# Kernel optimization log

Measured on AMD Instinct MI355X. Metric: run time of the kernel, lower is better.

Reference implementation:

```python
import jax, jax.numpy as jnp
import numpy as np


def setup_inputs() -> dict:
    key = jax.random.key(0)
    ks = jax.random.split(key, 8)
    C = 256
    Cq = C // 8  # 32
    B, H, W = 4, 64, 64
    x = jax.random.normal(ks[0], (B, C, H, W), dtype=jnp.float32)
    wq = jax.random.normal(ks[1], (Cq, C), dtype=jnp.float32) * (1.0 / np.sqrt(C))
    bq = jax.random.normal(ks[2], (Cq,), dtype=jnp.float32) * 0.01
    wk = jax.random.normal(ks[3], (Cq, C), dtype=jnp.float32) * (1.0 / np.sqrt(C))
    bk = jax.random.normal(ks[4], (Cq,), dtype=jnp.float32) * 0.01
    wv = jax.random.normal(ks[5], (C, C), dtype=jnp.float32) * (1.0 / np.sqrt(C))
    bv = jax.random.normal(ks[6], (C,), dtype=jnp.float32) * 0.01
    gamma = jax.random.normal(ks[7], (1,), dtype=jnp.float32)
    return {"x": x, "wq": wq, "bq": bq, "wk": wk, "bk": bk,
            "wv": wv, "bv": bv, "gamma": gamma}


def reference(x, wq, bq, wk, bk, wv, bv, gamma):
    B, C, H, W = x.shape
    N = H * W
    xf = x.reshape(B, C, N)  # [B, C, N] flattened spatial
    # 1x1 convs == per-position linear projections
    q = jnp.einsum('oc,bcn->bno', wq, xf) + bq          # [B, N, Cq]
    k = jnp.einsum('oc,bcn->bon', wk, xf) + bk[:, None]  # [B, Cq, N]
    v = jnp.einsum('oc,bcn->bon', wv, xf) + bv[:, None]  # [B, C, N]
    attn = jax.nn.softmax(jnp.einsum('bnc,bcm->bnm', q, k), axis=-1)  # [B, N, N]
    # out[b,c,n] = sum_m v[b,c,m] * attn[n,m]
    out = jnp.einsum('bcm,bnm->bcn', v, attn).reshape(B, C, H, W)
    return gamma[0] * out + x
```

## Files before the change

### kernel.cpp

```cpp
#include <hip/hip_runtime.h>

#define BB 4
#define CC 256
#define CQ 32
#define NN 4096

#define QT_OFF 0
#define KT_OFF (BB*NN*CQ)
#define VT_OFF (2*BB*NN*CQ)
#define WB_OFF (VT_OFF + BB*CC*NN)
#define BIAS_OFF (WB_OFF + 320*256)

typedef __attribute__((ext_vector_type(8))) short bf16x8;
typedef __attribute__((ext_vector_type(4))) short bf16x4;
typedef __attribute__((ext_vector_type(4))) float f32x4;

__device__ inline unsigned short f2bf(float f) {
    unsigned int u = __float_as_uint(f);
    u += 0x7fffu + ((u >> 16) & 1u);
    return (unsigned short)(u >> 16);
}

__global__ __launch_bounds__(256) void prepw_kernel(
    const float* __restrict__ wq, const float* __restrict__ bq,
    const float* __restrict__ wk, const float* __restrict__ bk,
    const float* __restrict__ wv, const float* __restrict__ bv,
    unsigned short* __restrict__ ws)
{
    unsigned short* Wb = ws + WB_OFF;
    float* Bias = (float*)(ws + BIAS_OFF);
    int idx = blockIdx.x * 256 + threadIdx.x;
    if (idx < 320 * 256) {
        int row = idx >> 8, col = idx & 255;
        float v = row < 32 ? wq[row * 256 + col]
                : row < 64 ? wk[(row - 32) * 256 + col]
                           : wv[(row - 64) * 256 + col];
        Wb[idx] = f2bf(v);
    }
    if (idx < 320)
        Bias[idx] = idx < 32 ? bq[idx] : idx < 64 ? bk[idx - 32] : bv[idx - 64];
}

__global__ __launch_bounds__(256, 2) void qkv_kernel(
    const float* __restrict__ x, unsigned short* __restrict__ ws)
{
    __shared__ __align__(16) unsigned short xs[32][264];
    __shared__ __align__(16) unsigned short vs[256][40];
    const int t = threadIdx.x;
    const int w = t >> 6, l = t & 63, quad = l >> 4, lc = l & 15;
    const int b = blockIdx.y, n0 = blockIdx.x * 32;

    unsigned short* qT = ws + QT_OFF;
    unsigned short* kT = ws + KT_OFF;
    const unsigned short* Wb = ws + WB_OFF;
    const float* Bias = (const float*)(ws + BIAS_OFF);

    const float* xb = x + (size_t)(b * CC) * NN + n0;
    {
        const int nq = t & 7, swz = (nq & 3) << 3;
#pragma unroll
        for (int p = 0; p < 8; ++p) {
            int c = p * 32 + (t >> 3);
            float4 v4 = *(const float4*)&xb[(size_t)c * NN + nq * 4];
            int cs = c ^ swz;
            xs[nq * 4 + 0][cs] = f2bf(v4.x);
            xs[nq * 4 + 1][cs] = f2bf(v4.y);
            xs[nq * 4 + 2][cs] = f2bf(v4.z);
            xs[nq * 4 + 3][cs] = f2bf(v4.w);
        }
    }
    __syncthreads();

    f32x4 acc[5][2];
#pragma unroll
    for (int j = 0; j < 5; ++j) {
        f32x4 b4 = *(const f32x4*)&Bias[(w * 5 + j) * 16 + quad * 4];
#pragma unroll
        for (int nt = 0; nt < 2; ++nt) acc[j][nt] = b4;
    }

#pragma unroll
    for (int s = 0; s < 8; ++s) {
        bf16x8 Af[5], Bf[2];
#pragma unroll
        for (int j = 0; j < 5; ++j)
            Af[j] = *(const bf16x8*)&Wb[((w * 5 + j) * 16 + lc) * 256 + s * 32 + quad * 8];
#pragma unroll
        for (int nt = 0; nt < 2; ++nt) {
            int pos = nt * 16 + lc;
            int col = (s * 32 + quad * 8) ^ (((pos >> 2) & 3) << 3);
            Bf[nt] = *(const bf16x8*)&xs[pos][col];
        }
#pragma unroll
        for (int j = 0; j < 5; ++j)
#pragma unroll
            for (int nt = 0; nt < 2; ++nt)
                acc[j][nt] = __builtin_amdgcn_mfma_f32_16x16x32_bf16(Af[j], Bf[nt], acc[j][nt], 0, 0, 0);
    }

#pragma unroll
    for (int j = 0; j < 5; ++j) {
        int ot = w * 5 + j;
#pragma unroll
        for (int nt = 0; nt < 2; ++nt) {
            if (ot < 4) {
                bf16x4 pk;
#pragma unroll
                for (int i = 0; i < 4; ++i) pk[i] = (short)f2bf(acc[j][nt][i]);
                unsigned short* bas = (ot < 2 ? qT : kT);
                int ocl = (ot & 1) * 16 + quad * 4;
                *(bf16x4*)&bas[((size_t)(b * NN + n0 + nt * 16 + lc)) * CQ + ocl] = pk;
            } else {
#pragma unroll
                for (int i = 0; i < 4; ++i)
                    vs[(ot - 4) * 16 + quad * 4 + i][nt * 16 + lc] = f2bf(acc[j][nt][i]);
            }
        }
    }
    __syncthreads();

    const int mt = n0 >> 6, hb = (n0 >> 5) & 1;
    unsigned short* vt = ws + VT_OFF + ((size_t)(b * 64 + mt) * 16) * 1024 + hb * 512;
#pragma unroll
    for (int p = 0; p < 4; ++p) {
        int ci = p * 256 + t;
        int ct = ci >> 6, g = (ci >> 4) & 3, lcp = ci & 15;
        bf16x8 chunk = *(const bf16x8*)&vs[ct * 16 + lcp][g * 8];
        *(bf16x8*)&vt[(size_t)ct * 1024 + g * 128 + lcp * 8] = chunk;
    }
}

__global__ __launch_bounds__(512, 2) void attn_kernel(
    const float* __restrict__ x, const unsigned short* __restrict__ ws,
    const float* __restrict__ gamma, float* __restrict__ out)
{
    __shared__ __align__(16) unsigned short Ps[2][64][136];
    __shared__ __align__(16) float lSpart[2][64];

    const int t = threadIdx.x;
    const int w = t >> 6, l = t & 63, quad = l >> 4, lc = l & 15;
    const int id = blockIdx.x, xcd = id & 7;
    const int b = xcd >> 1;
    const int n0 = (((id >> 3) << 1) | (xcd & 1)) * 64;

    const int qg = w & 3;
    const int kh = w >> 2;
    const int cb = w * 32;

    const unsigned short* qT = ws + QT_OFF;
    const unsigned short* kb = ws + KT_OFF + (size_t)b * NN * CQ;
    const unsigned short* vb = ws + VT_OFF + (size_t)b * 64 * 16 * 1024;

    const bf16x8 bq =
        *(const bf16x8*)&qT[((size_t)(b * NN + n0 + qg * 16 + lc)) * CQ + quad * 8];

    bf16x8 kA[4], kB[4];
    auto loadK = [&](bf16x8* kr, int tt) {
        int m0 = (tt & 31) * 128 + kh * 64;
#pragma unroll
        for (int j = 0; j < 4; ++j)
            kr[j] = *(const bf16x8*)&kb[(size_t)(m0 + j * 16 + lc) * CQ + quad * 8];
    };

    bf16x8 vA[2][4], vB[2][4];
    auto loadV = [&](bf16x8 (*vr)[4], int tt) {
#pragma unroll
        for (int c = 0; c < 2; ++c) {
            int ct = w * 2 + c;
#pragma unroll
            for (int k4 = 0; k4 < 4; ++k4) {
                int mt = (tt * 2 + (k4 >> 1)) & 63;
                vr[c][k4] = *(const bf16x8*)&vb[((size_t)mt * 16 + ct) * 1024 + (k4 & 1) * 512 + l * 8];
            }
        }
    };

    f32x4 acc[4][2];
#pragma unroll
    for (int i = 0; i < 4; ++i)
#pragma unroll
        for (int j = 0; j < 2; ++j) acc[i][j] = (f32x4){0.f, 0.f, 0.f, 0.f};

    f32x4 sn[4];
    float lacc = 0.f;
    const f32x4 z = {0.f, 0.f, 0.f, 0.f};

    auto expstore = [&](int pp) {
#pragma unroll
        for (int j = 0; j < 4; ++j) {
            bf16x4 pk;
#pragma unroll
            for (int i = 0; i < 4; ++i) {
                float p = __expf(sn[j][i]);
                lacc += p;
                pk[i] = (short)f2bf(p);
            }
            *(bf16x4*)&Ps[pp][qg * 16 + lc][kh * 64 + j * 16 + quad * 4] = pk;
        }
    };

    auto pv = [&](int pp, bf16x8 (*vr)[4]) {
#pragma unroll
        for (int ks = 0; ks < 4; ++ks)
#pragma unroll
            for (int qs = 0; qs < 4; ++qs) {
                bf16x8 ap = *(const bf16x8*)&Ps[pp][qs * 16 + lc][ks * 32 + quad * 8];
#pragma unroll
                for (int c = 0; c < 2; ++c)
                    acc[qs][c] = __builtin_amdgcn_mfma_f32_16x16x32_bf16(ap, vr[c][ks], acc[qs][c], 0, 0, 0);
            }
    };

    auto body = [&](int tt, int pp, bf16x8* kUse, bf16x8* kNext,
                    bf16x8 (*vUse)[4], bf16x8 (*vNext)[4]) {
        loadV(vNext, tt + 1);
#pragma unroll
        for (int j = 0; j < 4; ++j)
            sn[j] = __builtin_amdgcn_mfma_f32_16x16x32_bf16(kUse[j], bq, z, 0, 0, 0);
        loadK(kNext, tt + 2);
        expstore(pp ^ 1);
        pv(pp, vUse);
        __syncthreads();
    };

    loadK(kA, 0);
#pragma unroll
    for (int j = 0; j < 4; ++j)
        sn[j] = __builtin_amdgcn_mfma_f32_16x16x32_bf16(kA[j], bq, z, 0, 0, 0);
    loadK(kA, 1);
    expstore(0);
    loadV(vA, 0);
    __syncthreads();

    for (int it = 0; it < 15; ++it) {
        body(2 * it,     0, kA, kB, vA, vB);
        body(2 * it + 1, 1, kB, kA, vB, vA);
    }
    body(30, 0, kA, kB, vA, vB);
    pv(1, vB);

    lacc += __shfl_xor(lacc, 16);
    lacc += __shfl_xor(lacc, 32);
    if (quad == 0) lSpart[kh][qg * 16 + lc] = lacc;
    __syncthreads();

    const float g = gamma[0];
#pragma unroll
    for (int qs = 0; qs < 4; ++qs) {
        f32x4 l0 = *(const f32x4*)&lSpart[0][qs * 16 + quad * 4];
        f32x4 l1 = *(const f32x4*)&lSpart[1][qs * 16 + quad * 4];
        f32x4 rl;
#pragma unroll
        for (int i = 0; i < 4; ++i) rl[i] = 1.f / (l0[i] + l1[i]);
#pragma unroll
        for (int c2 = 0; c2 < 2; ++c2) {
            int c = cb + c2 * 16 + lc;
            size_t base = ((size_t)(b * CC + c)) * NN + n0 + qs * 16 + quad * 4;
            f32x4 xr = *(const f32x4*)&x[base];
            f32x4 o;
#pragma unroll
            for (int i = 0; i < 4; ++i) o[i] = g * acc[qs][c2][i] * rl[i] + xr[i];
            *(f32x4*)&out[base] = o;
        }
    }
}

extern "C" void kernel_launch(void* const* d_in, const int* in_sizes, int n_in,
                              void* d_out, int out_size, void* d_ws, size_t ws_size,
                              hipStream_t stream) {
    const float* x     = (const float*)d_in[0];
    const float* wq    = (const float*)d_in[1];
    const float* bq    = (const float*)d_in[2];
    const float* wk    = (const float*)d_in[3];
    const float* bk    = (const float*)d_in[4];
    const float* wv    = (const float*)d_in[5];
    const float* bv    = (const float*)d_in[6];
    const float* gamma = (const float*)d_in[7];
    float* out = (float*)d_out;
    unsigned short* ws = (unsigned short*)d_ws;

    prepw_kernel<<<320, 256, 0, stream>>>(wq, bq, wk, bk, wv, bv, ws);
    dim3 g1(NN / 32, BB);
    qkv_kernel<<<g1, 256, 0, stream>>>(x, ws);
    attn_kernel<<<256, 512, 0, stream>>>(x, ws, gamma, out);
}
```

Baseline: 145.8 us.

## Fuse QKV projection into attention kernel with per-tile global readiness flags

Merges the QKV projection and attention kernels into one persistent-style kernel. Each block projects its own 64-position tile, keeps Q in shared memory, and publishes K and V to global memory. It then signals per-tile flags and spins on the flags of the tiles it is about to consume, so attention can start before all projections finish. This removes a kernel launch and the global round trip for Q. The cost is spin-waits and a correctness dependence on all 256 blocks being co-resident.

Result: slower. 160.3 us (+9.9%).

```diff
diff --git a/kernel.cpp b/kernel.cpp
--- a/kernel.cpp
+++ b/kernel.cpp
@@ -5,11 +5,11 @@
 #define CQ 32
 #define NN 4096
 
-#define QT_OFF 0
-#define KT_OFF (BB*NN*CQ)
-#define VT_OFF (2*BB*NN*CQ)
+#define KT_OFF 0
+#define VT_OFF (BB*NN*CQ)
 #define WB_OFF (VT_OFF + BB*CC*NN)
 #define BIAS_OFF (WB_OFF + 320*256)
+#define FLAG_OFF (BIAS_OFF + 640)
 
 typedef __attribute__((ext_vector_type(8))) short bf16x8;
 typedef __attribute__((ext_vector_type(4))) short bf16x4;
@@ -19,6 +19,11 @@
     unsigned int u = __float_as_uint(f);
     u += 0x7fffu + ((u >> 16) & 1u);
     return (unsigned short)(u >> 16);
+}
+
+__device__ inline void spin_flag(int* p) {
+    while (__hip_atomic_load(p, __ATOMIC_RELAXED, __HIP_MEMORY_SCOPE_AGENT) == 0)
+        __builtin_amdgcn_s_sleep(1);
 }
 
 __global__ __launch_bounds__(256) void prepw_kernel(
@@ -29,6 +34,7 @@
 {
     unsigned short* Wb = ws + WB_OFF;
     float* Bias = (float*)(ws + BIAS_OFF);
+    int* flags = (int*)(ws + FLAG_OFF);
     int idx = blockIdx.x * 256 + threadIdx.x;
     if (idx < 320 * 256) {
         int row = idx >> 8, col = idx & 255;
@@ -39,28 +45,43 @@
     }
     if (idx < 320)
         Bias[idx] = idx < 32 ? bq[idx] : idx < 64 ? bk[idx - 32] : bv[idx - 64];
-}
-
-__global__ __launch_bounds__(256, 2) void qkv_kernel(
-    const float* __restrict__ x, unsigned short* __restrict__ ws)
+    if (idx < 260) flags[idx] = 0;
+}
+
+__global__ __launch_bounds__(512, 2) void fused_kernel(
+    const float* __restrict__ x, unsigned short* __restrict__ ws,
+    const float* __restrict__ gamma, float* __restrict__ out)
 {
-    __shared__ __align__(16) unsigned short xs[32][264];
-    __shared__ __align__(16) unsigned short vs[256][40];
+    __shared__ __align__(16) unsigned char smem[43008];
+    unsigned short (*xs)[264] = (unsigned short(*)[264])smem;
+    unsigned short (*vs)[72]  = (unsigned short(*)[72])smem;
+    unsigned short (*qsh)[40] = (unsigned short(*)[40])(smem + 36864);
+    unsigned short (*Ps)[64][136] = (unsigned short(*)[64][136])smem;
+    float* lSpart = (float*)(smem + 41984);
+    int* aRdy = (int*)(smem + 42496);
+
     const int t = threadIdx.x;
     const int w = t >> 6, l = t & 63, quad = l >> 4, lc = l & 15;
-    const int b = blockIdx.y, n0 = blockIdx.x * 32;
-
-    unsigned short* qT = ws + QT_OFF;
+    const int id = blockIdx.x, xcd = id & 7;
+    const int b = xcd >> 1;
+    const int n0 = (((id >> 3) << 1) | (xcd & 1)) * 64;
+    const int mt64 = n0 >> 6;
+
     unsigned short* kT = ws + KT_OFF;
+    unsigned short* vT = ws + VT_OFF;
     const unsigned short* Wb = ws + WB_OFF;
     const float* Bias = (const float*)(ws + BIAS_OFF);
-
-    const float* xb = x + (size_t)(b * CC) * NN + n0;
+    int* flags = (int*)(ws + FLAG_OFF);
+    int* bdone = flags + 256;
+
+    if (t == 0) *aRdy = 0;
+
     {
-        const int nq = t & 7, swz = (nq & 3) << 3;
+        const float* xb = x + (size_t)(b * CC) * NN + n0;
+        const int nq = t & 15, swz = (nq & 3) << 3;
 #pragma unroll
         for (int p = 0; p < 8; ++p) {
-            int c = p * 32 + (t >> 3);
+            int c = p * 32 + (t >> 4);
             float4 v4 = *(const float4*)&xb[(size_t)c * NN + nq * 4];
             int cs = c ^ swz;
             xs[nq * 4 + 0][cs] = f2bf(v4.x);
@@ -68,91 +89,87 @@
             xs[nq * 4 + 2][cs] = f2bf(v4.z);
             xs[nq * 4 + 3][cs] = f2bf(v4.w);
         }
-    }
-    __syncthreads();
-
-    f32x4 acc[5][2];
-#pragma unroll
-    for (int j = 0; j < 5; ++j) {
-        f32x4 b4 = *(const f32x4*)&Bias[(w * 5 + j) * 16 + quad * 4];
-#pragma unroll
-        for (int nt = 0; nt < 2; ++nt) acc[j][nt] = b4;
-    }
-
-#pragma unroll
-    for (int s = 0; s < 8; ++s) {
-        bf16x8 Af[5], Bf[2];
-#pragma unroll
-        for (int j = 0; j < 5; ++j)
-            Af[j] = *(const bf16x8*)&Wb[((w * 5 + j) * 16 + lc) * 256 + s * 32 + quad * 8];
-#pragma unroll
-        for (int nt = 0; nt < 2; ++nt) {
-            int pos = nt * 16 + lc;
-            int col = (s * 32 + quad * 8) ^ (((pos >> 2) & 3) << 3);
-            Bf[nt] = *(const bf16x8*)&xs[pos][col];
-        }
-#pragma unroll
-        for (int j = 0; j < 5; ++j)
-#pragma unroll
-            for (int nt = 0; nt < 2; ++nt)
-                acc[j][nt] = __builtin_amdgcn_mfma_f32_16x16x32_bf16(Af[j], Bf[nt], acc[j][nt], 0, 0, 0);
-    }
-
-#pragma unroll
-    for (int j = 0; j < 5; ++j) {
-        int ot = w * 5 + j;
-#pragma unroll
-        for (int nt = 0; nt < 2; ++nt) {
-            if (ot < 4) {
-                bf16x4 pk;
-#pragma unroll
-                for (int i = 0; i < 4; ++i) pk[i] = (short)f2bf(acc[j][nt][i]);
-                unsigned short* bas = (ot < 2 ? qT : kT);
-                int ocl = (ot & 1) * 16 + quad * 4;
-                *(bf16x4*)&bas[((size_t)(b * NN + n0 + nt * 16 + lc)) * CQ + ocl] = pk;
-            } else {
-#pragma unroll
-                for (int i = 0; i < 4; ++i)
-                    vs[(ot - 4) * 16 + quad * 4 + i][nt * 16 + lc] = f2bf(acc[j][nt][i]);
-            }
-        }
-    }
-    __syncthreads();
-
-    const int mt = n0 >> 6, hb = (n0 >> 5) & 1;
-    unsigned short* vt = ws + VT_OFF + ((size_t)(b * 64 + mt) * 16) * 1024 + hb * 512;
-#pragma unroll
-    for (int p = 0; p < 4; ++p) {
-        int ci = p * 256 + t;
-        int ct = ci >> 6, g = (ci >> 4) & 3, lcp = ci & 15;
-        bf16x8 chunk = *(const bf16x8*)&vs[ct * 16 + lcp][g * 8];
-        *(bf16x8*)&vt[(size_t)ct * 1024 + g * 128 + lcp * 8] = chunk;
-    }
-}
-
-__global__ __launch_bounds__(512, 2) void attn_kernel(
-    const float* __restrict__ x, const unsigned short* __restrict__ ws,
-    const float* __restrict__ gamma, float* __restrict__ out)
-{
-    __shared__ __align__(16) unsigned short Ps[2][64][136];
-    __shared__ __align__(16) float lSpart[2][64];
-
-    const int t = threadIdx.x;
-    const int w = t >> 6, l = t & 63, quad = l >> 4, lc = l & 15;
-    const int id = blockIdx.x, xcd = id & 7;
-    const int b = xcd >> 1;
-    const int n0 = (((id >> 3) << 1) | (xcd & 1)) * 64;
+        __syncthreads();
+
+        const int pr = w >> 1, nh = w & 1;
+        f32x4 acc[5][2];
+#pragma unroll
+        for (int j = 0; j < 5; ++j) {
+            f32x4 b4 = *(const f32x4*)&Bias[(pr * 5 + j) * 16 + quad * 4];
+            acc[j][0] = b4; acc[j][1] = b4;
+        }
+#pragma unroll
+        for (int s = 0; s < 8; ++s) {
+            bf16x8 Af[5], Bf[2];
+#pragma unroll
+            for (int j = 0; j < 5; ++j)
+                Af[j] = *(const bf16x8*)&Wb[((pr * 5 + j) * 16 + lc) * 256 + s * 32 + quad * 8];
+#pragma unroll
+            for (int n2 = 0; n2 < 2; ++n2) {
+                int pos = (nh * 2 + n2) * 16 + lc;
+                int col = (s * 32 + quad * 8) ^ (((pos >> 2) & 3) << 3);
+                Bf[n2] = *(const bf16x8*)&xs[pos][col];
+            }
+#pragma unroll
+            for (int j = 0; j < 5; ++j)
+#pragma unroll
+                for (int n2 = 0; n2 < 2; ++n2)
+                    acc[j][n2] = __builtin_amdgcn_mfma_f32_16x16x32_bf16(Af[j], Bf[n2], acc[j][n2], 0, 0, 0);
+        }
+        __syncthreads();
+
+#pragma unroll
+        for (int j = 0; j < 5; ++j) {
+            int ot = pr * 5 + j;
+#pragma unroll
+            for (int n2 = 0; n2 < 2; ++n2) {
+                int pos = (nh * 2 + n2) * 16 + lc;
+                if (ot < 2) {
+#pragma unroll
+                    for (int i = 0; i < 4; ++i)
+                        qsh[pos][ot * 16 + quad * 4 + i] = f2bf(acc[j][n2][i]);
+                } else if (ot < 4) {
+                    bf16x4 pk;
+#pragma unroll
+                    for (int i = 0; i < 4; ++i) pk[i] = (short)f2bf(acc[j][n2][i]);
+                    *(bf16x4*)&kT[((size_t)(b * NN + n0 + pos)) * CQ + (ot - 2) * 16 + quad * 4] = pk;
+                } else {
+#pragma unroll
+                    for (int i = 0; i < 4; ++i)
+                        vs[(ot - 4) * 16 + quad * 4 + i][pos] = f2bf(acc[j][n2][i]);
+                }
+            }
+        }
+        __syncthreads();
+
+        unsigned short* vtile = vT + ((size_t)(b * 64 + mt64)) * 16384;
+#pragma unroll
+        for (int p = 0; p < 4; ++p) {
+            int ci = p * 512 + t;
+            int ct = ci >> 7, ks = (ci >> 6) & 1, ln = ci & 63;
+            int q2 = ln >> 4, lc2 = ln & 15;
+            bf16x8 chunk = *(const bf16x8*)&vs[ct * 16 + lc2][ks * 32 + q2 * 8];
+            *(bf16x8*)&vtile[(size_t)ct * 1024 + ks * 512 + ln * 8] = chunk;
+        }
+    }
 
     const int qg = w & 3;
     const int kh = w >> 2;
     const int cb = w * 32;
 
-    const unsigned short* qT = ws + QT_OFF;
-    const unsigned short* kb = ws + KT_OFF + (size_t)b * NN * CQ;
-    const unsigned short* vb = ws + VT_OFF + (size_t)b * 64 * 16 * 1024;
-
-    const bf16x8 bq =
-        *(const bf16x8*)&qT[((size_t)(b * NN + n0 + qg * 16 + lc)) * CQ + quad * 8];
+    __syncthreads();
+    const bf16x8 bqf = *(const bf16x8*)&qsh[qg * 16 + lc][quad * 8];
+
+    if (t == 0) {
+        __threadfence();
+        atomicAdd(&flags[b * 64 + mt64], 1);
+        atomicAdd(&bdone[b], 1);
+    }
+    if (t < 6) spin_flag(&flags[b * 64 + t]);
+    __syncthreads();
+
+    const unsigned short* kb = kT + (size_t)b * NN * CQ;
+    const unsigned short* vb = vT + ((size_t)b << 20);
 
     bf16x8 kA[4], kB[4];
     auto loadK = [&](bf16x8* kr, int tt) {
@@ -161,7 +178,6 @@
         for (int j = 0; j < 4; ++j)
             kr[j] = *(const bf16x8*)&kb[(size_t)(m0 + j * 16 + lc) * CQ + quad * 8];
     };
-
     bf16x8 vA[2][4], vB[2][4];
     auto loadV = [&](bf16x8 (*vr)[4], int tt) {
 #pragma unroll
@@ -169,18 +185,17 @@
             int ct = w * 2 + c;
 #pragma unroll
             for (int k4 = 0; k4 < 4; ++k4) {
-                int mt = (tt * 2 + (k4 >> 1)) & 63;
-                vr[c][k4] = *(const bf16x8*)&vb[((size_t)mt * 16 + ct) * 1024 + (k4 & 1) * 512 + l * 8];
-            }
-        }
-    };
-
-    f32x4 acc[4][2];
+                int m = ((tt & 31) * 2 + (k4 >> 1));
+                vr[c][k4] = *(const bf16x8*)&vb[((size_t)m * 16 + ct) * 1024 + (k4 & 1) * 512 + l * 8];
+            }
+        }
+    };
+
+    f32x4 acc2[4][2];
 #pragma unroll
     for (int i = 0; i < 4; ++i)
 #pragma unroll
-        for (int j = 0; j < 2; ++j) acc[i][j] = (f32x4){0.f, 0.f, 0.f, 0.f};
-
+        for (int j = 0; j < 2; ++j) acc2[i][j] = (f32x4){0.f, 0.f, 0.f, 0.f};
     f32x4 sn[4];
     float lacc = 0.f;
     const f32x4 z = {0.f, 0.f, 0.f, 0.f};
@@ -198,7 +213,6 @@
             *(bf16x4*)&Ps[pp][qg * 16 + lc][kh * 64 + j * 16 + quad * 4] = pk;
         }
     };
-
     auto pv = [&](int pp, bf16x8 (*vr)[4]) {
 #pragma unroll
         for (int ks = 0; ks < 4; ++ks)
@@ -207,7 +221,7 @@
                 bf16x8 ap = *(const bf16x8*)&Ps[pp][qs * 16 + lc][ks * 32 + quad * 8];
 #pragma unroll
                 for (int c = 0; c < 2; ++c)
-                    acc[qs][c] = __builtin_amdgcn_mfma_f32_16x16x32_bf16(ap, vr[c][ks], acc[qs][c], 0, 0, 0);
+                    acc2[qs][c] = __builtin_amdgcn_mfma_f32_16x16x32_bf16(ap, vr[c][ks], acc2[qs][c], 0, 0, 0);
             }
     };
 
@@ -216,17 +230,25 @@
         loadV(vNext, tt + 1);
 #pragma unroll
         for (int j = 0; j < 4; ++j)
-            sn[j] = __builtin_amdgcn_mfma_f32_16x16x32_bf16(kUse[j], bq, z, 0, 0, 0);
+            sn[j] = __builtin_amdgcn_mfma_f32_16x16x32_bf16(kUse[j], bqf, z, 0, 0, 0);
         loadK(kNext, tt + 2);
         expstore(pp ^ 1);
         pv(pp, vUse);
+        int nt3 = tt + 3;
+        if (nt3 <= 31 && t < 3) {
+            if (__hip_atomic_load(aRdy, __ATOMIC_RELAXED, __HIP_MEMORY_SCOPE_WORKGROUP) == 0) {
+                if (t < 2) spin_flag(&flags[b * 64 + nt3 * 2 + t]);
+                else if (__hip_atomic_load(&bdone[b], __ATOMIC_RELAXED, __HIP_MEMORY_SCOPE_AGENT) == 64)
+                    *aRdy = 1;
+            }
+        }
         __syncthreads();
     };
 
     loadK(kA, 0);
 #pragma unroll
     for (int j = 0; j < 4; ++j)
-        sn[j] = __builtin_amdgcn_mfma_f32_16x16x32_bf16(kA[j], bq, z, 0, 0, 0);
+        sn[j] = __builtin_amdgcn_mfma_f32_16x16x32_bf16(kA[j], bqf, z, 0, 0, 0);
     loadK(kA, 1);
     expstore(0);
     loadV(vA, 0);
@@ -241,14 +263,14 @@
 
     lacc += __shfl_xor(lacc, 16);
     lacc += __shfl_xor(lacc, 32);
-    if (quad == 0) lSpart[kh][qg * 16 + lc] = lacc;
+    if (quad == 0) lSpart[kh * 64 + qg * 16 + lc] = lacc;
     __syncthreads();
 
     const float g = gamma[0];
 #pragma unroll
     for (int qs = 0; qs < 4; ++qs) {
-        f32x4 l0 = *(const f32x4*)&lSpart[0][qs * 16 + quad * 4];
-        f32x4 l1 = *(const f32x4*)&lSpart[1][qs * 16 + quad * 4];
+        f32x4 l0 = *(const f32x4*)&lSpart[qs * 16 + quad * 4];
+        f32x4 l1 = *(const f32x4*)&lSpart[64 + qs * 16 + quad * 4];
         f32x4 rl;
 #pragma unroll
         for (int i = 0; i < 4; ++i) rl[i] = 1.f / (l0[i] + l1[i]);
@@ -259,7 +281,7 @@
             f32x4 xr = *(const f32x4*)&x[base];
             f32x4 o;
 #pragma unroll
-            for (int i = 0; i < 4; ++i) o[i] = g * acc[qs][c2][i] * rl[i] + xr[i];
+            for (int i = 0; i < 4; ++i) o[i] = g * acc2[qs][c2][i] * rl[i] + xr[i];
             *(f32x4*)&out[base] = o;
         }
     }
@@ -280,7 +302,5 @@
     unsigned short* ws = (unsigned short*)d_ws;
 
     prepw_kernel<<<320, 256, 0, stream>>>(wq, bq, wk, bk, wv, bv, ws);
-    dim3 g1(NN / 32, BB);
-    qkv_kernel<<<g1, 256, 0, stream>>>(x, ws);
-    attn_kernel<<<256, 512, 0, stream>>>(x, ws, gamma, out);
-}
+    fused_kernel<<<256, 512, 0, stream>>>(x, ws, gamma, out);
+}
```
